# Optimization experiments

Hardware: AMD Instinct MI355X
Metric: run time of the kernel (lower is better)

Reference implementation:

```python
import jax, jax.numpy as jnp
import numpy as np

EPS = 1e-12  # F.normalize eps


def _l2norm(v, axis):
    n = jnp.sqrt(jnp.sum(v * v, axis=axis, keepdims=True))
    return v / jnp.maximum(n, EPS)


def setup_inputs() -> dict:
    key = jax.random.key(0)
    k1, k2, k3, k4 = jax.random.split(key, 4)
    N, C, H, W = 48, 512, 40, 40
    K = 64
    x = jax.random.normal(k1, (N, C, H, W), dtype=jnp.float32)
    conv_w = jax.random.normal(k2, (K, C), dtype=jnp.float32) * 0.02   # cluster-assign 1x1 conv, no bias (vladv2=False)
    attn_w = jax.random.normal(k3, (1, C), dtype=jnp.float32) * 0.02   # heatmap 1x1 conv
    attn_b = jnp.zeros((1,), dtype=jnp.float32)
    centroids = jax.random.uniform(k4, (K, C), dtype=jnp.float32)      # torch.rand init
    return {"x": x, "conv_w": conv_w, "attn_w": attn_w, "attn_b": attn_b, "centroids": centroids}


def reference(x, conv_w, attn_w, attn_b, centroids):
    N, C, H, W = x.shape
    K = conv_w.shape[0]
    P = H * W

    # attention heatmap: ReLU -> 1x1 conv -> ReLU  => [N, 1, H, W]
    hmp = jax.nn.relu(jnp.einsum('nchw,oc->nohw', jax.nn.relu(x), attn_w) + attn_b[None, :, None, None])
    hmp_flat = hmp.reshape(N, 1, P)  # [N,1,P]

    # normalize input descriptors across channels
    xn = _l2norm(x, axis=1)                      # [N,C,H,W]
    x_flat = xn.reshape(N, C, P)                 # [N,C,P]

    # soft assignment: 1x1 conv over clusters + softmax over cluster dim
    logits = jnp.einsum('ncp,kc->nkp', x_flat, conv_w)   # [N,K,P]
    soft_assign = jax.nn.softmax(logits, axis=1)          # softmax over K

    # weighted residual aggregation, fused:
    # vlad[n,k,c] = sum_p (x[n,c,p] - centroids[k,c]) * sa[n,k,p] * hmp[n,0,p]
    w = soft_assign * hmp_flat                            # [N,K,P]
    term1 = jnp.einsum('nkp,ncp->nkc', w, x_flat)         # [N,K,C]
    wsum = jnp.sum(w, axis=-1)                            # [N,K]
    vlad = term1 - wsum[:, :, None] * centroids[None, :, :]

    vlad = _l2norm(vlad, axis=2)                          # intra-normalize per cluster
    vlad = vlad.reshape(N, K * C)
    vlad = _l2norm(vlad, axis=1)                          # global L2 normalize
    return vlad
```

## Files before the change

kernel.cpp:

```cpp
#include <hip/hip_runtime.h>
#include <math.h>

#define NN 48
#define CC 512
#define KK 64
#define PP 1600
#define EPSF 1e-12f

typedef short short8 __attribute__((ext_vector_type(8)));
typedef float f32x4 __attribute__((ext_vector_type(4)));

static __device__ __forceinline__ unsigned short f2bf(float f) {
    unsigned u = __float_as_uint(f);
    u += 0x7fffu + ((u >> 16) & 1u);
    return (unsigned short)(u >> 16);
}
static __device__ __forceinline__ unsigned pack2(float a, float b) {
    return (unsigned)f2bf(a) | ((unsigned)f2bf(b) << 16);
}

__global__ __launch_bounds__(256, 4) void kn_logits(
    const float* __restrict__ x, const float* __restrict__ conv_w,
    const float* __restrict__ attn_w, const float* __restrict__ attn_b,
    unsigned short* __restrict__ wg, float* __restrict__ wsum)
{
    __shared__ unsigned short xt[64][76];
    __shared__ unsigned short cwb[64][72];
    __shared__ float attn_l[CC];
    __shared__ float red[16][64];
    __shared__ float invn_l[64];
    __shared__ float hmp_l[64];
    __shared__ float wsum_l[KK];

    const int n = blockIdx.y, p0 = blockIdx.x * 64, tid = threadIdx.x;
    const int q = tid & 15, cg = tid >> 4;
    const int wave = tid >> 6, lane = tid & 63;
    const int lq = lane >> 4, lm = lane & 15;
    const int kr = tid >> 2, cq = tid & 3;

    for (int i = tid; i < CC; i += 256) attn_l[i] = attn_w[i];
    if (tid < KK) wsum_l[tid] = 0.f;

    f32x4 acc[4];
#pragma unroll
    for (int mt = 0; mt < 4; ++mt) acc[mt] = (f32x4){0.f, 0.f, 0.f, 0.f};
    float ss[4] = {0.f, 0.f, 0.f, 0.f};
    float ad[4] = {0.f, 0.f, 0.f, 0.f};

    const float* xb = x + (size_t)n * CC * PP;
    const float* wp0 = conv_w + (size_t)kr * CC + cq * 16;
    const float* xp0 = xb + (size_t)(cg * 4) * PP + p0 + 4 * q;

    float4 wv[4], xv[4];
#pragma unroll
    for (int j = 0; j < 4; ++j) wv[j] = *(const float4*)(wp0 + 4 * j);
#pragma unroll
    for (int j = 0; j < 4; ++j) xv[j] = *(const float4*)(xp0 + (size_t)j * PP);

    __syncthreads();

#pragma unroll 1
    for (int cs = 0; cs < 8; ++cs) {
        float4 wn[4], xn_[4];
        if (cs < 7) {
            const float* wp = wp0 + (cs + 1) * 64;
            const float* xp = xp0 + (size_t)(cs + 1) * 64 * PP;
#pragma unroll
            for (int j = 0; j < 4; ++j) wn[j] = *(const float4*)(wp + 4 * j);
#pragma unroll
            for (int j = 0; j < 4; ++j) xn_[j] = *(const float4*)(xp + (size_t)j * PP);
        }
#pragma unroll
        for (int j = 0; j < 4; ++j) {
            uint2 u = {pack2(wv[j].x, wv[j].y), pack2(wv[j].z, wv[j].w)};
            *(uint2*)&cwb[kr][cq * 16 + 4 * j] = u;
        }
        const int cbase = cs * 64 + cg * 4;
#pragma unroll
        for (int j = 0; j < 4; ++j) {
            float4 v = xv[j];
            const float aw = attn_l[cbase + j];
            ss[0] += v.x * v.x; ss[1] += v.y * v.y;
            ss[2] += v.z * v.z; ss[3] += v.w * v.w;
            ad[0] += fmaxf(v.x, 0.f) * aw; ad[1] += fmaxf(v.y, 0.f) * aw;
            ad[2] += fmaxf(v.z, 0.f) * aw; ad[3] += fmaxf(v.w, 0.f) * aw;
            uint2 u = {pack2(v.x, v.y), pack2(v.z, v.w)};
            *(uint2*)&xt[cg * 4 + j][4 * q] = u;
        }
        __syncthreads();
#pragma unroll
        for (int ks = 0; ks < 2; ++ks) {
            short8 af[4];
#pragma unroll
            for (int mt = 0; mt < 4; ++mt)
                af[mt] = *(const short8*)&cwb[mt * 16 + lm][ks * 32 + lq * 8];
            const int pl = wave * 16 + lm;
            const int cb = ks * 32 + lq * 8;
            short8 bv;
#pragma unroll
            for (int j = 0; j < 8; ++j) bv[j] = (short)xt[cb + j][pl];
#pragma unroll
            for (int mt = 0; mt < 4; ++mt)
                acc[mt] = __builtin_amdgcn_mfma_f32_16x16x32_bf16(
                    af[mt], bv, acc[mt], 0, 0, 0);
        }
        __syncthreads();
        if (cs < 7) {
#pragma unroll
            for (int j = 0; j < 4; ++j) { wv[j] = wn[j]; xv[j] = xn_[j]; }
        }
    }

#pragma unroll
    for (int j = 0; j < 4; ++j) red[cg][4 * q + j] = ss[j];
    __syncthreads();
    if (tid < 64) {
        float S = 0.f;
#pragma unroll
        for (int l = 0; l < 16; ++l) S += red[l][tid];
        invn_l[tid] = 1.f / fmaxf(sqrtf(S), EPSF);
    }
    __syncthreads();
#pragma unroll
    for (int j = 0; j < 4; ++j) red[cg][4 * q + j] = ad[j];
    __syncthreads();
    if (tid < 64) {
        float A = 0.f;
#pragma unroll
        for (int l = 0; l < 16; ++l) A += red[l][tid];
        hmp_l[tid] = fmaxf(A + attn_b[0], 0.f);
    }
    __syncthreads();

    const int pl = wave * 16 + lm;
    const float inv = invn_l[pl];
    const float hp = hmp_l[pl];
    float mx = -1e30f;
#pragma unroll
    for (int mt = 0; mt < 4; ++mt)
#pragma unroll
        for (int r = 0; r < 4; ++r) {
            const float l = acc[mt][r] * inv;
            acc[mt][r] = l;
            mx = fmaxf(mx, l);
        }
    mx = fmaxf(mx, __shfl_xor(mx, 16));
    mx = fmaxf(mx, __shfl_xor(mx, 32));
    float s = 0.f;
#pragma unroll
    for (int mt = 0; mt < 4; ++mt)
#pragma unroll
        for (int r = 0; r < 4; ++r) {
            const float e = __expf(acc[mt][r] - mx);
            acc[mt][r] = e;
            s += e;
        }
    s += __shfl_xor(s, 16);
    s += __shfl_xor(s, 32);
    const float sden = hp / s;

    unsigned short* wrb = wg + (size_t)n * KK * PP + p0;
#pragma unroll
    for (int mt = 0; mt < 4; ++mt)
#pragma unroll
        for (int r = 0; r < 4; ++r) {
            const int k = mt * 16 + lq * 4 + r;
            const float w0 = acc[mt][r] * sden;
            float wk = w0;
#pragma unroll
            for (int o = 1; o < 16; o <<= 1) wk += __shfl_xor(wk, o);
            if (lm == 0) atomicAdd(&wsum_l[k], wk);
            wrb[(size_t)k * PP + pl] = f2bf(w0 * inv);
        }
    __syncthreads();
    if (tid < KK) atomicAdd(&wsum[n * KK + tid], wsum_l[tid]);
}

__global__ __launch_bounds__(256) void kn_term1(
    const float* __restrict__ xf, const unsigned short* __restrict__ wgq,
    float* __restrict__ term1p)
{
    __shared__ unsigned short wt[64][40];
    __shared__ unsigned short xt2[64][40];
    const int c0 = blockIdx.x * 64, n = blockIdx.y, ph = blockIdx.z;
    const int tid = threadIdx.x;
    const int wave = tid >> 6, lane = tid & 63, lq = lane >> 4, lm = lane & 15;
    const int koff = (wave >> 1) * 32, coff = (wave & 1) * 32;
    const int s_begin = (50 * ph) >> 2, s_end = (50 * (ph + 1)) >> 2;
    const int rA = tid >> 2, cq = tid & 3;

    f32x4 acc[2][2];
#pragma unroll
    for (int mt = 0; mt < 2; ++mt)
#pragma unroll
        for (int nt = 0; nt < 2; ++nt) acc[mt][nt] = (f32x4){0.f, 0.f, 0.f, 0.f};

    const unsigned short* wb = wgq + (size_t)n * KK * PP + (size_t)rA * PP + cq * 8;
    const float* xfb = xf + ((size_t)n * CC + c0 + rA) * PP + cq * 8;

    auto ldB = [&](int p) -> uint4 {
        const float* sp = xfb + p;
        float4 a = *(const float4*)sp, b = *(const float4*)(sp + 4);
        return make_uint4(pack2(a.x, a.y), pack2(a.z, a.w),
                          pack2(b.x, b.y), pack2(b.z, b.w));
    };

    uint4 pa = *(const uint4*)(wb + s_begin * 32);
    uint4 pb = ldB(s_begin * 32);

    for (int ps = s_begin; ps < s_end; ++ps) {
        uint4 na, nb;
        if (ps + 1 < s_end) {
            na = *(const uint4*)(wb + (ps + 1) * 32);
            nb = ldB((ps + 1) * 32);
        }
        *(uint4*)&wt[rA][cq * 8] = pa;
        *(uint4*)&xt2[rA][cq * 8] = pb;
        __syncthreads();
        short8 af[2], bv[2];
#pragma unroll
        for (int mt = 0; mt < 2; ++mt)
            af[mt] = *(const short8*)&wt[koff + mt * 16 + lm][lq * 8];
#pragma unroll
        for (int nt = 0; nt < 2; ++nt)
            bv[nt] = *(const short8*)&xt2[coff + nt * 16 + lm][lq * 8];
#pragma unroll
        for (int mt = 0; mt < 2; ++mt)
#pragma unroll
            for (int nt = 0; nt < 2; ++nt)
                acc[mt][nt] = __builtin_amdgcn_mfma_f32_16x16x32_bf16(
                    af[mt], bv[nt], acc[mt][nt], 0, 0, 0);
        __syncthreads();
        pa = na; pb = nb;
    }

    float* ob = term1p + ((size_t)ph * NN + n) * KK * CC + c0 + coff;
#pragma unroll
    for (int mt = 0; mt < 2; ++mt)
#pragma unroll
        for (int r = 0; r < 4; ++r) {
            const int k = koff + mt * 16 + lq * 4 + r;
#pragma unroll
            for (int nt = 0; nt < 2; ++nt)
                ob[(size_t)k * CC + nt * 16 + lm] = acc[mt][nt][r];
        }
}

__global__ __launch_bounds__(128) void kn_vlad(
    const float* __restrict__ term1p, const float* __restrict__ wsum,
    const float* __restrict__ cent, float* __restrict__ out)
{
    const int k = blockIdx.x, n = blockIdx.y, tid = threadIdx.x;
    const size_t base = ((size_t)n * KK + k) * CC;
    const size_t NKC = (size_t)NN * KK * CC;
    const float ws = wsum[n * KK + k];
    const int c = tid * 4;

    float4 ce = *(const float4*)(cent + (size_t)k * CC + c);
    float4 v = {-ws * ce.x, -ws * ce.y, -ws * ce.z, -ws * ce.w};
#pragma unroll
    for (int h = 0; h < 4; ++h) {
        float4 a = *(const float4*)(term1p + h * NKC + base + c);
        v.x += a.x; v.y += a.y; v.z += a.z; v.w += a.w;
    }

    float s = v.x * v.x + v.y * v.y + v.z * v.z + v.w * v.w;
#pragma unroll
    for (int o = 32; o >= 1; o >>= 1) s += __shfl_down(s, o, 64);

    __shared__ float rb[2];
    __shared__ float sinv;
    if ((tid & 63) == 0) rb[tid >> 6] = s;
    __syncthreads();
    if (tid == 0) {
        const float S = rb[0] + rb[1];
        sinv = 0.125f / fmaxf(sqrtf(S), EPSF);
    }
    __syncthreads();
    const float inv = sinv;
    float4 o4 = {v.x * inv, v.y * inv, v.z * inv, v.w * inv};
    *(float4*)(out + base + c) = o4;
}

extern "C" void kernel_launch(void* const* d_in, const int* in_sizes, int n_in,
                              void* d_out, int out_size, void* d_ws, size_t ws_size,
                              hipStream_t stream)
{
    (void)in_sizes; (void)n_in; (void)out_size; (void)ws_size;
    const float* x      = (const float*)d_in[0];
    const float* conv_w = (const float*)d_in[1];
    const float* attn_w = (const float*)d_in[2];
    const float* attn_b = (const float*)d_in[3];
    const float* cent   = (const float*)d_in[4];
    float* out = (float*)d_out;

    char* w = (char*)d_ws;
    float* term1p = (float*)w;            w += (size_t)4 * NN * KK * CC * 4;
    float* wsum   = (float*)w;            w += (size_t)NN * KK * 4;
    unsigned short* wg = (unsigned short*)w;

    hipMemsetAsync(wsum, 0, NN * KK * sizeof(float), stream);

    kn_logits<<<dim3(25, NN), 256, 0, stream>>>(x, conv_w, attn_w, attn_b,
                                                wg, wsum);
    kn_term1<<<dim3(8, NN, 4), 256, 0, stream>>>(x, wg, term1p);
    kn_vlad <<<dim3(KK, NN), 128, 0, stream>>>(term1p, wsum, cent, out);
}
```

Baseline: 300.8 us.

## Fuse logits/softmax and term1 GEMM into one kernel, reading x once

Merges the soft-assignment kernel and the weighted aggregation GEMM into one kernel. Each block processes a 320-pixel span of one image in 32-pixel slices, keeps the bf16 x slice in LDS and reuses it for both MFMA GEMMs. A small prep kernel pre-converts conv_w to bf16, and the block holds its A fragments in registers. This removes the second read of x and the global round trip of the weight matrix. The cost is only 240 large blocks and many barriers per slice, so there is less latency hiding.

```diff
diff --git a/kernel.cpp b/kernel.cpp
--- a/kernel.cpp
+++ b/kernel.cpp
@@ -5,6 +5,10 @@
 #define CC 512
 #define KK 64
 #define PP 1600
+#define PH 5
+#define PBLK 320
+#define SL 32
+#define NSL 10
 #define EPSF 1e-12f
 
 typedef short short8 __attribute__((ext_vector_type(8)));
@@ -19,231 +23,170 @@
     return (unsigned)f2bf(a) | ((unsigned)f2bf(b) << 16);
 }
 
-__global__ __launch_bounds__(256, 4) void kn_logits(
-    const float* __restrict__ x, const float* __restrict__ conv_w,
+__global__ __launch_bounds__(512) void kn_prep(
+    const float* __restrict__ conv_w, unsigned short* __restrict__ cwb_g)
+{
+    const int idx = blockIdx.x * 512 + threadIdx.x;
+    cwb_g[idx] = f2bf(conv_w[idx]);
+}
+
+__global__ __launch_bounds__(512, 2) void kn_fused(
+    const float* __restrict__ x, const unsigned short* __restrict__ cwb_g,
     const float* __restrict__ attn_w, const float* __restrict__ attn_b,
-    unsigned short* __restrict__ wg, float* __restrict__ wsum)
-{
-    __shared__ unsigned short xt[64][76];
-    __shared__ unsigned short cwb[64][72];
+    float* __restrict__ wsum, float* __restrict__ term1p)
+{
+    __shared__ unsigned short xall[512][32];
+    __shared__ unsigned short wlds[64][32];
+    __shared__ float red_ss[64][32];
+    __shared__ float red_ad[64][32];
+    __shared__ float smx[32][4], ssm[32][4];
+    __shared__ float invn_l[32], hmp_l[32];
+    __shared__ float wsum_l[KK];
     __shared__ float attn_l[CC];
-    __shared__ float red[16][64];
-    __shared__ float invn_l[64];
-    __shared__ float hmp_l[64];
-    __shared__ float wsum_l[KK];
-
-    const int n = blockIdx.y, p0 = blockIdx.x * 64, tid = threadIdx.x;
-    const int q = tid & 15, cg = tid >> 4;
-    const int wave = tid >> 6, lane = tid & 63;
+
+    const int ph = blockIdx.x, n = blockIdx.y, tid = threadIdx.x;
+    const int wv = tid >> 6, lane = tid & 63;
     const int lq = lane >> 4, lm = lane & 15;
-    const int kr = tid >> 2, cq = tid & 3;
-
-    for (int i = tid; i < CC; i += 256) attn_l[i] = attn_w[i];
-    if (tid < KK) wsum_l[tid] = 0.f;
-
-    f32x4 acc[4];
-#pragma unroll
-    for (int mt = 0; mt < 4; ++mt) acc[mt] = (f32x4){0.f, 0.f, 0.f, 0.f};
-    float ss[4] = {0.f, 0.f, 0.f, 0.f};
-    float ad[4] = {0.f, 0.f, 0.f, 0.f};
-
-    const float* xb = x + (size_t)n * CC * PP;
-    const float* wp0 = conv_w + (size_t)kr * CC + cq * 16;
-    const float* xp0 = xb + (size_t)(cg * 4) * PP + p0 + 4 * q;
-
-    float4 wv[4], xv[4];
-#pragma unroll
-    for (int j = 0; j < 4; ++j) wv[j] = *(const float4*)(wp0 + 4 * j);
-#pragma unroll
-    for (int j = 0; j < 4; ++j) xv[j] = *(const float4*)(xp0 + (size_t)j * PP);
+    const int kt = wv >> 1, ph2 = wv & 1;
+    const int pl = ph2 * 16 + lm;
+    const int kb = wv >> 2, cb = wv & 3;
+    const int sr = tid >> 3, sq = tid & 7;
+
+    attn_l[tid] = attn_w[tid];
+    if (tid >= 512 - KK) wsum_l[tid - (512 - KK)] = 0.f;
+    const float ab = attn_b[0];
+
+    f32x4 acc2[2][8];
+#pragma unroll
+    for (int mt = 0; mt < 2; ++mt)
+#pragma unroll
+        for (int nt = 0; nt < 8; ++nt) acc2[mt][nt] = (f32x4){0.f, 0.f, 0.f, 0.f};
+
+    const float* xb = x + (size_t)n * CC * PP + ph * PBLK;
+    const unsigned short* afb = cwb_g + (size_t)(kt * 16 + lm) * CC;
+    short8 af_all[16];
+#pragma unroll
+    for (int t = 0; t < 16; ++t)
+        af_all[t] = *(const short8*)(afb + t * 32 + lq * 8);
 
     __syncthreads();
 
-#pragma unroll 1
-    for (int cs = 0; cs < 8; ++cs) {
-        float4 wn[4], xn_[4];
-        if (cs < 7) {
-            const float* wp = wp0 + (cs + 1) * 64;
-            const float* xp = xp0 + (size_t)(cs + 1) * 64 * PP;
-#pragma unroll
-            for (int j = 0; j < 4; ++j) wn[j] = *(const float4*)(wp + 4 * j);
-#pragma unroll
-            for (int j = 0; j < 4; ++j) xn_[j] = *(const float4*)(xp + (size_t)j * PP);
-        }
-#pragma unroll
-        for (int j = 0; j < 4; ++j) {
-            uint2 u = {pack2(wv[j].x, wv[j].y), pack2(wv[j].z, wv[j].w)};
-            *(uint2*)&cwb[kr][cq * 16 + 4 * j] = u;
-        }
-        const int cbase = cs * 64 + cg * 4;
-#pragma unroll
-        for (int j = 0; j < 4; ++j) {
-            float4 v = xv[j];
-            const float aw = attn_l[cbase + j];
+    for (int sl = 0; sl < NSL; ++sl) {
+        const int ps = sl * SL;
+        float ss[4] = {0.f, 0.f, 0.f, 0.f};
+        float ad[4] = {0.f, 0.f, 0.f, 0.f};
+        float4 xv[8];
+#pragma unroll
+        for (int cs = 0; cs < 8; ++cs)
+            xv[cs] = *(const float4*)(xb + (size_t)(cs * 64 + sr) * PP + ps + sq * 4);
+#pragma unroll
+        for (int cs = 0; cs < 8; ++cs) {
+            const float4 v = xv[cs];
+            const float aw = attn_l[cs * 64 + sr];
             ss[0] += v.x * v.x; ss[1] += v.y * v.y;
             ss[2] += v.z * v.z; ss[3] += v.w * v.w;
             ad[0] += fmaxf(v.x, 0.f) * aw; ad[1] += fmaxf(v.y, 0.f) * aw;
             ad[2] += fmaxf(v.z, 0.f) * aw; ad[3] += fmaxf(v.w, 0.f) * aw;
             uint2 u = {pack2(v.x, v.y), pack2(v.z, v.w)};
-            *(uint2*)&xt[cg * 4 + j][4 * q] = u;
-        }
-        __syncthreads();
-#pragma unroll
-        for (int ks = 0; ks < 2; ++ks) {
-            short8 af[4];
-#pragma unroll
-            for (int mt = 0; mt < 4; ++mt)
-                af[mt] = *(const short8*)&cwb[mt * 16 + lm][ks * 32 + lq * 8];
-            const int pl = wave * 16 + lm;
-            const int cb = ks * 32 + lq * 8;
+            *(uint2*)&xall[cs * 64 + sr][sq * 4] = u;
+        }
+#pragma unroll
+        for (int j = 0; j < 4; ++j) {
+            red_ss[sr][sq * 4 + j] = ss[j];
+            red_ad[sr][sq * 4 + j] = ad[j];
+        }
+        __syncthreads();
+
+        if (tid < 32) {
+            float S = 0.f;
+#pragma unroll 8
+            for (int g = 0; g < 64; ++g) S += red_ss[g][tid];
+            invn_l[tid] = 1.f / fmaxf(sqrtf(S), EPSF);
+        } else if (tid < 64) {
+            const int p = tid - 32;
+            float A = 0.f;
+#pragma unroll 8
+            for (int g = 0; g < 64; ++g) A += red_ad[g][p];
+            hmp_l[p] = fmaxf(A + ab, 0.f);
+        }
+        __syncthreads();
+
+        f32x4 a1 = (f32x4){0.f, 0.f, 0.f, 0.f};
+#pragma unroll
+        for (int t = 0; t < 16; ++t) {
+            const int cb8 = t * 32 + lq * 8;
             short8 bv;
 #pragma unroll
-            for (int j = 0; j < 8; ++j) bv[j] = (short)xt[cb + j][pl];
-#pragma unroll
-            for (int mt = 0; mt < 4; ++mt)
-                acc[mt] = __builtin_amdgcn_mfma_f32_16x16x32_bf16(
-                    af[mt], bv, acc[mt], 0, 0, 0);
-        }
-        __syncthreads();
-        if (cs < 7) {
-#pragma unroll
-            for (int j = 0; j < 4; ++j) { wv[j] = wn[j]; xv[j] = xn_[j]; }
-        }
+            for (int j = 0; j < 8; ++j) bv[j] = (short)xall[cb8 + j][pl];
+            a1 = __builtin_amdgcn_mfma_f32_16x16x32_bf16(af_all[t], bv, a1, 0, 0, 0);
+        }
+
+        const float inv = invn_l[pl], hp = hmp_l[pl];
+        float l0[4];
+        float mxw = -1e30f;
+#pragma unroll
+        for (int r = 0; r < 4; ++r) {
+            l0[r] = a1[r] * inv;
+            mxw = fmaxf(mxw, l0[r]);
+        }
+        mxw = fmaxf(mxw, __shfl_xor(mxw, 16));
+        mxw = fmaxf(mxw, __shfl_xor(mxw, 32));
+        if (lq == 0) smx[pl][kt] = mxw;
+        __syncthreads();
+        const float mx = fmaxf(fmaxf(smx[pl][0], smx[pl][1]),
+                               fmaxf(smx[pl][2], smx[pl][3]));
+        float e[4];
+        float sw = 0.f;
+#pragma unroll
+        for (int r = 0; r < 4; ++r) {
+            e[r] = __expf(l0[r] - mx);
+            sw += e[r];
+        }
+        sw += __shfl_xor(sw, 16);
+        sw += __shfl_xor(sw, 32);
+        if (lq == 0) ssm[pl][kt] = sw;
+        __syncthreads();
+        const float s = ssm[pl][0] + ssm[pl][1] + ssm[pl][2] + ssm[pl][3];
+        const float sden = hp / s;
+
+#pragma unroll
+        for (int r = 0; r < 4; ++r) {
+            const float w0 = e[r] * sden;
+            float wk = w0;
+#pragma unroll
+            for (int o = 1; o < 16; o <<= 1) wk += __shfl_xor(wk, o);
+            if (lm == 0) atomicAdd(&wsum_l[kt * 16 + lq * 4 + r], wk);
+            wlds[kt * 16 + lq * 4 + r][pl] = f2bf(w0 * inv);
+        }
+        __syncthreads();
+
+        short8 af2[2], bv2[8];
+#pragma unroll
+        for (int mt = 0; mt < 2; ++mt)
+            af2[mt] = *(const short8*)&wlds[kb * 32 + mt * 16 + lm][lq * 8];
+#pragma unroll
+        for (int nt = 0; nt < 8; ++nt)
+            bv2[nt] = *(const short8*)&xall[cb * 128 + nt * 16 + lm][lq * 8];
+#pragma unroll
+        for (int mt = 0; mt < 2; ++mt)
+#pragma unroll
+            for (int nt = 0; nt < 8; ++nt)
+                acc2[mt][nt] = __builtin_amdgcn_mfma_f32_16x16x32_bf16(
+                    af2[mt], bv2[nt], acc2[mt][nt], 0, 0, 0);
+        __syncthreads();
     }
 
-#pragma unroll
-    for (int j = 0; j < 4; ++j) red[cg][4 * q + j] = ss[j];
-    __syncthreads();
-    if (tid < 64) {
-        float S = 0.f;
-#pragma unroll
-        for (int l = 0; l < 16; ++l) S += red[l][tid];
-        invn_l[tid] = 1.f / fmaxf(sqrtf(S), EPSF);
-    }
-    __syncthreads();
-#pragma unroll
-    for (int j = 0; j < 4; ++j) red[cg][4 * q + j] = ad[j];
-    __syncthreads();
-    if (tid < 64) {
-        float A = 0.f;
-#pragma unroll
-        for (int l = 0; l < 16; ++l) A += red[l][tid];
-        hmp_l[tid] = fmaxf(A + attn_b[0], 0.f);
-    }
-    __syncthreads();
-
-    const int pl = wave * 16 + lm;
-    const float inv = invn_l[pl];
-    const float hp = hmp_l[pl];
-    float mx = -1e30f;
-#pragma unroll
-    for (int mt = 0; mt < 4; ++mt)
-#pragma unroll
-        for (int r = 0; r < 4; ++r) {
-            const float l = acc[mt][r] * inv;
-            acc[mt][r] = l;
-            mx = fmaxf(mx, l);
-        }
-    mx = fmaxf(mx, __shfl_xor(mx, 16));
-    mx = fmaxf(mx, __shfl_xor(mx, 32));
-    float s = 0.f;
-#pragma unroll
-    for (int mt = 0; mt < 4; ++mt)
-#pragma unroll
-        for (int r = 0; r < 4; ++r) {
-            const float e = __expf(acc[mt][r] - mx);
-            acc[mt][r] = e;
-            s += e;
-        }
-    s += __shfl_xor(s, 16);
-    s += __shfl_xor(s, 32);
-    const float sden = hp / s;
-
-    unsigned short* wrb = wg + (size_t)n * KK * PP + p0;
-#pragma unroll
-    for (int mt = 0; mt < 4; ++mt)
-#pragma unroll
-        for (int r = 0; r < 4; ++r) {
-            const int k = mt * 16 + lq * 4 + r;
-            const float w0 = acc[mt][r] * sden;
-            float wk = w0;
-#pragma unroll
-            for (int o = 1; o < 16; o <<= 1) wk += __shfl_xor(wk, o);
-            if (lm == 0) atomicAdd(&wsum_l[k], wk);
-            wrb[(size_t)k * PP + pl] = f2bf(w0 * inv);
-        }
-    __syncthreads();
+    float* ob = term1p + ((size_t)ph * NN + n) * KK * CC;
+#pragma unroll
+    for (int mt = 0; mt < 2; ++mt)
+#pragma unroll
+        for (int r = 0; r < 4; ++r) {
+            const int k = kb * 32 + mt * 16 + lq * 4 + r;
+#pragma unroll
+            for (int nt = 0; nt < 8; ++nt)
+                ob[(size_t)k * CC + cb * 128 + nt * 16 + lm] = acc2[mt][nt][r];
+        }
     if (tid < KK) atomicAdd(&wsum[n * KK + tid], wsum_l[tid]);
-}
-
-__global__ __launch_bounds__(256) void kn_term1(
-    const float* __restrict__ xf, const unsigned short* __restrict__ wgq,
-    float* __restrict__ term1p)
-{
-    __shared__ unsigned short wt[64][40];
-    __shared__ unsigned short xt2[64][40];
-    const int c0 = blockIdx.x * 64, n = blockIdx.y, ph = blockIdx.z;
-    const int tid = threadIdx.x;
-    const int wave = tid >> 6, lane = tid & 63, lq = lane >> 4, lm = lane & 15;
-    const int koff = (wave >> 1) * 32, coff = (wave & 1) * 32;
-    const int s_begin = (50 * ph) >> 2, s_end = (50 * (ph + 1)) >> 2;
-    const int rA = tid >> 2, cq = tid & 3;
-
-    f32x4 acc[2][2];
-#pragma unroll
-    for (int mt = 0; mt < 2; ++mt)
-#pragma unroll
-        for (int nt = 0; nt < 2; ++nt) acc[mt][nt] = (f32x4){0.f, 0.f, 0.f, 0.f};
-
-    const unsigned short* wb = wgq + (size_t)n * KK * PP + (size_t)rA * PP + cq * 8;
-    const float* xfb = xf + ((size_t)n * CC + c0 + rA) * PP + cq * 8;
-
-    auto ldB = [&](int p) -> uint4 {
-        const float* sp = xfb + p;
-        float4 a = *(const float4*)sp, b = *(const float4*)(sp + 4);
-        return make_uint4(pack2(a.x, a.y), pack2(a.z, a.w),
-                          pack2(b.x, b.y), pack2(b.z, b.w));
-    };
-
-    uint4 pa = *(const uint4*)(wb + s_begin * 32);
-    uint4 pb = ldB(s_begin * 32);
-
-    for (int ps = s_begin; ps < s_end; ++ps) {
-        uint4 na, nb;
-        if (ps + 1 < s_end) {
-            na = *(const uint4*)(wb + (ps + 1) * 32);
-            nb = ldB((ps + 1) * 32);
-        }
-        *(uint4*)&wt[rA][cq * 8] = pa;
-        *(uint4*)&xt2[rA][cq * 8] = pb;
-        __syncthreads();
-        short8 af[2], bv[2];
-#pragma unroll
-        for (int mt = 0; mt < 2; ++mt)
-            af[mt] = *(const short8*)&wt[koff + mt * 16 + lm][lq * 8];
-#pragma unroll
-        for (int nt = 0; nt < 2; ++nt)
-            bv[nt] = *(const short8*)&xt2[coff + nt * 16 + lm][lq * 8];
-#pragma unroll
-        for (int mt = 0; mt < 2; ++mt)
-#pragma unroll
-            for (int nt = 0; nt < 2; ++nt)
-                acc[mt][nt] = __builtin_amdgcn_mfma_f32_16x16x32_bf16(
-                    af[mt], bv[nt], acc[mt][nt], 0, 0, 0);
-        __syncthreads();
-        pa = na; pb = nb;
-    }
-
-    float* ob = term1p + ((size_t)ph * NN + n) * KK * CC + c0 + coff;
-#pragma unroll
-    for (int mt = 0; mt < 2; ++mt)
-#pragma unroll
-        for (int r = 0; r < 4; ++r) {
-            const int k = koff + mt * 16 + lq * 4 + r;
-#pragma unroll
-            for (int nt = 0; nt < 2; ++nt)
-                ob[(size_t)k * CC + nt * 16 + lm] = acc[mt][nt][r];
-        }
 }
 
 __global__ __launch_bounds__(128) void kn_vlad(
@@ -259,7 +202,7 @@
     float4 ce = *(const float4*)(cent + (size_t)k * CC + c);
     float4 v = {-ws * ce.x, -ws * ce.y, -ws * ce.z, -ws * ce.w};
 #pragma unroll
-    for (int h = 0; h < 4; ++h) {
+    for (int h = 0; h < PH; ++h) {
         float4 a = *(const float4*)(term1p + h * NKC + base + c);
         v.x += a.x; v.y += a.y; v.z += a.z; v.w += a.w;
     }
@@ -295,14 +238,14 @@
     float* out = (float*)d_out;
 
     char* w = (char*)d_ws;
-    float* term1p = (float*)w;            w += (size_t)4 * NN * KK * CC * 4;
-    float* wsum   = (float*)w;            w += (size_t)NN * KK * 4;
-    unsigned short* wg = (unsigned short*)w;
+    float* term1p = (float*)w;            w += (size_t)PH * NN * KK * CC * 4;
+    float* wsum   = (float*)w;            w += ((size_t)NN * KK * 4 + 255) & ~255ULL;
+    unsigned short* cwb_g = (unsigned short*)w;
 
     hipMemsetAsync(wsum, 0, NN * KK * sizeof(float), stream);
 
-    kn_logits<<<dim3(25, NN), 256, 0, stream>>>(x, conv_w, attn_w, attn_b,
-                                                wg, wsum);
-    kn_term1<<<dim3(8, NN, 4), 256, 0, stream>>>(x, wg, term1p);
+    kn_prep <<<dim3(KK * CC / 512), 512, 0, stream>>>(conv_w, cwb_g);
+    kn_fused<<<dim3(PH, NN), 512, 0, stream>>>(x, cwb_g, attn_w, attn_b,
+                                               wsum, term1p);
     kn_vlad <<<dim3(KK, NN), 128, 0, stream>>>(term1p, wsum, cent, out);
 }
```

After: 279.1 us. 7.2% less time.
